# Kernel optimization log

Hardware: AMD Instinct MI355X
Metric: run time of the kernel (lower is better)

## Reference

```python
import jax, jax.numpy as jnp
import numpy as np

QUERY_DIM = 1024
KEY_DIM = 512
HIDDEN_DIM = 128
BATCH = 32
SEQ_LEN = 2048


def setup_inputs() -> dict:
    key = jax.random.key(0)
    k1, k2, k3, k4, k5 = jax.random.split(key, 5)
    query = jax.random.normal(k1, (BATCH, QUERY_DIM), dtype=jnp.float32)
    keys = jax.random.normal(k2, (BATCH, SEQ_LEN, KEY_DIM), dtype=jnp.float32)
    # nn.Linear weights, stored as (out, in) like torch; scaled ~ kaiming-uniform bound
    W1 = jax.random.normal(k3, (HIDDEN_DIM, QUERY_DIM), dtype=jnp.float32) / np.sqrt(QUERY_DIM)
    W2 = jax.random.normal(k4, (HIDDEN_DIM, KEY_DIM), dtype=jnp.float32) / np.sqrt(KEY_DIM)
    V = jax.random.normal(k5, (1, HIDDEN_DIM), dtype=jnp.float32) / np.sqrt(HIDDEN_DIM)
    return {"query": query, "keys": keys, "W1": W1, "W2": W2, "V": V}


def reference(query, keys, W1, W2, V):
    # query: [b, q], keys: [b, s, k]
    q_proj = jnp.einsum("bq,hq->bh", query, W1)          # [b, h]
    k_proj = jnp.einsum("bsk,hk->bsh", keys, W2)          # [b, s, h]
    hidden = jnp.tanh(q_proj[:, None, :] + k_proj)        # [b, s, h]
    score = jnp.einsum("bsh,oh->bs", hidden, V)           # [b, s] (o == 1)
    attention_weights = jax.nn.softmax(score, axis=1)     # [b, s]
    context = jnp.einsum("bs,bsk->bk", attention_weights, keys)  # [b, k]
    return (context, attention_weights)
```

## Files before the change

### kernel.cpp

```cpp
#include <hip/hip_runtime.h>

#define BATCH 32
#define SEQ   2048
#define KD    512
#define QD    1024
#define HD    128

#define NT 16
#define ROWS 64
#define NCHUNK 32

typedef float    f32x4 __attribute__((ext_vector_type(4)));
typedef _Float16 f16x8 __attribute__((ext_vector_type(8)));
typedef unsigned int u32;

__device__ __forceinline__ u32 pack2h(float a, float b) {
    _Float16 ha = (_Float16)a, hb = (_Float16)b;
    unsigned short ua = __builtin_bit_cast(unsigned short, ha);
    unsigned short ub = __builtin_bit_cast(unsigned short, hb);
    return (u32)ua | ((u32)ub << 16);
}

__device__ __forceinline__ void cvt16(const f32x4 a[4], uint4& h0, uint4& h1) {
    h0 = make_uint4(pack2h(a[0][0], a[0][1]), pack2h(a[0][2], a[0][3]),
                    pack2h(a[1][0], a[1][1]), pack2h(a[1][2], a[1][3]));
    h1 = make_uint4(pack2h(a[2][0], a[2][1]), pack2h(a[2][2], a[2][3]),
                    pack2h(a[3][0], a[3][1]), pack2h(a[3][2], a[3][3]));
}

__device__ __forceinline__ f16x8 cvtA(const float4& r0, const float4& r1) {
    uint4 u = make_uint4(pack2h(r0.x, r0.y), pack2h(r0.z, r0.w),
                         pack2h(r1.x, r1.y), pack2h(r1.z, r1.w));
    return __builtin_bit_cast(f16x8, u);
}

__device__ __forceinline__ void gload_lds16(const void* g, void* l) {
    __builtin_amdgcn_global_load_lds(
        (const __attribute__((address_space(1))) unsigned int*)g,
        (__attribute__((address_space(3))) unsigned int*)l, 16, 0, 0);
}

__global__ __launch_bounds__(256) void prep_kernel(
        const float* __restrict__ query, const float* __restrict__ W1,
        const float* __restrict__ W2, float* __restrict__ qp,
        char* __restrict__ w2img) {
    int blk = blockIdx.x;
    int tid = threadIdx.x;
    if (blk < 512) {
        int b = blk >> 4, hg = blk & 15;
        int wave = tid >> 6, lane = tid & 63;
        int h = hg * 8 + wave * 2 + (lane >> 5);
        int l32 = lane & 31;
        const float* q = query + (size_t)b * QD;
        const float* w = W1 + (size_t)h * QD;
        float acc = 0.f;
        #pragma unroll
        for (int i = 0; i < 8; ++i) {
            float4 qv = *(const float4*)(q + i * 128 + l32 * 4);
            float4 wv = *(const float4*)(w + i * 128 + l32 * 4);
            acc += qv.x * wv.x + qv.y * wv.y + qv.z * wv.z + qv.w * wv.w;
        }
        #pragma unroll
        for (int off = 16; off >= 1; off >>= 1) acc += __shfl_xor(acc, off);
        if (l32 == 0) qp[b * HD + h] = acc;
    } else {
        int c = blk - 512;
        int row = tid >> 1;
        int scol = (tid & 1) * 16;
        const float* src = W2 + (size_t)row * KD + c * 32 + scol;
        f32x4 a[4];
        #pragma unroll
        for (int i = 0; i < 4; ++i) a[i] = *(const f32x4*)(src + i * 4);
        uint4 h0, h1;
        cvt16(a, h0, h1);
        int sw = (row & 7) << 4;
        int b0 = c * 8192 + ((row * 64 + scol * 2) ^ sw);
        int b1 = c * 8192 + ((row * 64 + scol * 2 + 16) ^ sw);
        *(uint4*)(w2img + b0) = h0;
        *(uint4*)(w2img + b1) = h1;
    }
}

__global__ __launch_bounds__(256, 4) void score_ctx_kernel(
        const float* __restrict__ keys, const char* __restrict__ w2img,
        const float* __restrict__ qp, const float* __restrict__ V,
        float* __restrict__ score_out, float* __restrict__ part_m,
        float* __restrict__ part_l, float* __restrict__ part_c) {
    __shared__ __align__(16) char Bl[2][8192];
    __shared__ float sc[ROWS];
    __shared__ float pb[ROWS];

    const int blk  = blockIdx.x;
    const int m0   = blk * ROWS;
    const int b    = blk >> 5;
    const int tid  = threadIdx.x;
    const int wave = tid >> 6;
    const int lane = tid & 63;
    const int l15  = lane & 15;
    const int l4   = lane >> 4;

    const float* arow = keys + (size_t)(m0 + wave * 16 + l15) * KD + l4 * 8;
    const int boff0 = (l15 * 64 + l4 * 16) ^ ((l15 & 7) << 4);

    f32x4 acc[8];
    #pragma unroll
    for (int hj = 0; hj < 8; ++hj) acc[hj] = (f32x4)0.f;

    float4 ka[2][2];

#define KA(slot, t) { \
        ka[slot][0] = *(const float4*)(arow + (t) * 32); \
        ka[slot][1] = *(const float4*)(arow + (t) * 32 + 4); }
#define BSTAGE(slot, t) { \
        const char* g_ = w2img + (t) * 8192 + wave * 2048 + lane * 16; \
        gload_lds16(g_,        &Bl[slot][wave * 2048]); \
        gload_lds16(g_ + 1024, &Bl[slot][wave * 2048 + 1024]); }

    BSTAGE(0, 0)
    KA(0, 0)
    __syncthreads();

    #pragma unroll
    for (int t = 0; t < NT; ++t) {
        const int cb = t & 1, nb = cb ^ 1;
        if (t + 1 < NT) {
            BSTAGE(nb, t + 1)
            KA(nb, t + 1)
        }
        f16x8 af = cvtA(ka[cb][0], ka[cb][1]);
        #pragma unroll
        for (int hj = 0; hj < 8; ++hj) {
            f16x8 bh = *(const f16x8*)(&Bl[cb][boff0 + hj * 1024]);
            acc[hj] = __builtin_amdgcn_mfma_f32_16x16x32_f16(af, bh, acc[hj], 0, 0, 0);
        }
        __syncthreads();
    }
#undef KA
#undef BSTAGE

    float qv[8], vv[8];
    #pragma unroll
    for (int hj = 0; hj < 8; ++hj) {
        qv[hj] = qp[b * HD + hj * 16 + l15];
        vv[hj] = V[hj * 16 + l15];
    }

    #pragma unroll
    for (int j = 0; j < 4; ++j) {
        float p = 0.f;
        #pragma unroll
        for (int hj = 0; hj < 8; ++hj) {
            float x = qv[hj] + acc[hj][j];
            float e = __expf(2.f * x);
            float th = 1.f - 2.f * __builtin_amdgcn_rcpf(1.f + e);
            p += th * vv[hj];
        }
        #pragma unroll
        for (int off = 1; off < 16; off <<= 1) p += __shfl_xor(p, off);
        if (l15 == 0) {
            int r = wave * 16 + l4 * 4 + j;
            score_out[m0 + r] = p;
            sc[r] = p;
        }
    }
    __syncthreads();

    float s_val = sc[lane];
    float mx = s_val;
    #pragma unroll
    for (int off = 32; off >= 1; off >>= 1) mx = fmaxf(mx, __shfl_xor(mx, off));
    float p = __expf(s_val - mx);
    float ls = p;
    #pragma unroll
    for (int off = 32; off >= 1; off >>= 1) ls += __shfl_xor(ls, off);
    if (wave == 0) pb[lane] = p;
    if (tid == 0) {
        part_m[blk] = mx;
        part_l[blk] = ls;
    }
    __syncthreads();

    int col = tid * 2;
    float c0 = 0.f, c1 = 0.f;
    const float* kb2 = keys + (size_t)m0 * KD + col;
    #pragma unroll 8
    for (int s = 0; s < ROWS; ++s) {
        float w = pb[s];
        float2 kv = *(const float2*)(kb2 + (size_t)s * KD);
        c0 = fmaf(w, kv.x, c0);
        c1 = fmaf(w, kv.y, c1);
    }
    *(float2*)(part_c + (size_t)blk * KD + col) = make_float2(c0, c1);
}

__global__ __launch_bounds__(256) void finalize_kernel(
        const float* __restrict__ part_m, const float* __restrict__ part_l,
        const float* __restrict__ part_c, float* __restrict__ ctx,
        float* __restrict__ wts) {
    __shared__ float eS[NCHUNK];
    int b = blockIdx.x;
    int tid = threadIdx.x;
    float M = -1e30f;
    #pragma unroll 8
    for (int i = 0; i < NCHUNK; ++i) M = fmaxf(M, part_m[b * NCHUNK + i]);
    if (tid < NCHUNK) eS[tid] = __expf(part_m[b * NCHUNK + tid] - M);
    __syncthreads();
    float L = 0.f;
    #pragma unroll 8
    for (int i = 0; i < NCHUNK; ++i) L += eS[i] * part_l[b * NCHUNK + i];
    float invL = 1.f / L;
    #pragma unroll
    for (int r = 0; r < 8; ++r) {
        int s = tid + r * 256;
        float scv = wts[b * SEQ + s];
        wts[b * SEQ + s] = __expf(scv - M) * invL;
    }
    int col = tid * 2;
    float c0 = 0.f, c1 = 0.f;
    #pragma unroll 8
    for (int i = 0; i < NCHUNK; ++i) {
        float w = eS[i];
        float2 pc = *(const float2*)(part_c + (size_t)(b * NCHUNK + i) * KD + col);
        c0 = fmaf(w, pc.x, c0);
        c1 = fmaf(w, pc.y, c1);
    }
    ctx[b * KD + col]     = c0 * invL;
    ctx[b * KD + col + 1] = c1 * invL;
}

extern "C" void kernel_launch(void* const* d_in, const int* in_sizes, int n_in,
                              void* d_out, int out_size, void* d_ws, size_t ws_size,
                              hipStream_t stream) {
    const float* query = (const float*)d_in[0];
    const float* keys  = (const float*)d_in[1];
    const float* W1    = (const float*)d_in[2];
    const float* W2    = (const float*)d_in[3];
    const float* V     = (const float*)d_in[4];

    float* ctx = (float*)d_out;
    float* wts = (float*)d_out + BATCH * KD;

    char* wsb     = (char*)d_ws;
    float* qp     = (float*)wsb;
    char*  w2img  = wsb + 16 * 1024;
    float* part_m = (float*)(wsb + 144 * 1024);
    float* part_l = (float*)(wsb + 148 * 1024);
    float* part_c = (float*)(wsb + 152 * 1024);

    prep_kernel<<<528, 256, 0, stream>>>(query, W1, W2, qp, w2img);
    score_ctx_kernel<<<BATCH * NCHUNK, 256, 0, stream>>>(
        keys, w2img, qp, V, wts, part_m, part_l, part_c);
    finalize_kernel<<<BATCH, 256, 0, stream>>>(part_m, part_l, part_c, ctx, wts);
}
```

Before: 58.06 us.

## Stage keys tiles through LDS with triple-buffered async loads and single barrier

The keys A-operand now goes global-to-LDS through async global_load_lds with an XOR swizzle, instead of sitting in a register double buffer. Keys and W2 tiles share a three-slot slab so one barrier per iteration is enough, gated by explicit vmcnt waits. The change also raises wave priority around the MFMA block and hoists the qp/V loads. The larger LDS footprint (48KB) lowers the occupancy target from 4 to 3 blocks per CU, and the hand-written waitcnt and barrier logic is fragile.

```diff
diff --git a/kernel.cpp b/kernel.cpp
--- a/kernel.cpp
+++ b/kernel.cpp
@@ -28,9 +28,9 @@
                     pack2h(a[3][0], a[3][1]), pack2h(a[3][2], a[3][3]));
 }
 
-__device__ __forceinline__ f16x8 cvtA(const float4& r0, const float4& r1) {
-    uint4 u = make_uint4(pack2h(r0.x, r0.y), pack2h(r0.z, r0.w),
-                         pack2h(r1.x, r1.y), pack2h(r1.z, r1.w));
+__device__ __forceinline__ f16x8 cvtA4(const f32x4& r0, const f32x4& r1) {
+    uint4 u = make_uint4(pack2h(r0[0], r0[1]), pack2h(r0[2], r0[3]),
+                         pack2h(r1[0], r1[1]), pack2h(r1[2], r1[3]));
     return __builtin_bit_cast(f16x8, u);
 }
 
@@ -81,12 +81,12 @@
     }
 }
 
-__global__ __launch_bounds__(256, 4) void score_ctx_kernel(
+__global__ __launch_bounds__(256, 3) void score_ctx_kernel(
         const float* __restrict__ keys, const char* __restrict__ w2img,
         const float* __restrict__ qp, const float* __restrict__ V,
         float* __restrict__ score_out, float* __restrict__ part_m,
         float* __restrict__ part_l, float* __restrict__ part_c) {
-    __shared__ __align__(16) char Bl[2][8192];
+    __shared__ __align__(16) char slab[3][16384];
     __shared__ float sc[ROWS];
     __shared__ float pb[ROWS];
 
@@ -99,51 +99,59 @@
     const int l15  = lane & 15;
     const int l4   = lane >> 4;
 
-    const float* arow = keys + (size_t)(m0 + wave * 16 + l15) * KD + l4 * 8;
-    const int boff0 = (l15 * 64 + l4 * 16) ^ ((l15 & 7) << 4);
-
-    f32x4 acc[8];
-    #pragma unroll
-    for (int hj = 0; hj < 8; ++hj) acc[hj] = (f32x4)0.f;
-
-    float4 ka[2][2];
-
-#define KA(slot, t) { \
-        ka[slot][0] = *(const float4*)(arow + (t) * 32); \
-        ka[slot][1] = *(const float4*)(arow + (t) * 32 + 4); }
-#define BSTAGE(slot, t) { \
-        const char* g_ = w2img + (t) * 8192 + wave * 2048 + lane * 16; \
-        gload_lds16(g_,        &Bl[slot][wave * 2048]); \
-        gload_lds16(g_ + 1024, &Bl[slot][wave * 2048 + 1024]); }
-
-    BSTAGE(0, 0)
-    KA(0, 0)
-    __syncthreads();
-
-    #pragma unroll
-    for (int t = 0; t < NT; ++t) {
-        const int cb = t & 1, nb = cb ^ 1;
-        if (t + 1 < NT) {
-            BSTAGE(nb, t + 1)
-            KA(nb, t + 1)
-        }
-        f16x8 af = cvtA(ka[cb][0], ka[cb][1]);
-        #pragma unroll
-        for (int hj = 0; hj < 8; ++hj) {
-            f16x8 bh = *(const f16x8*)(&Bl[cb][boff0 + hj * 1024]);
-            acc[hj] = __builtin_amdgcn_mfma_f32_16x16x32_f16(af, bh, acc[hj], 0, 0, 0);
-        }
-        __syncthreads();
-    }
-#undef KA
-#undef BSTAGE
-
     float qv[8], vv[8];
     #pragma unroll
     for (int hj = 0; hj < 8; ++hj) {
         qv[hj] = qp[b * HD + hj * 16 + l15];
         vv[hj] = V[hj * 16 + l15];
     }
+
+    const char* asrc0 = (const char*)keys
+        + (size_t)(m0 + wave * 16 + (lane >> 3)) * (KD * 4)
+        + (((lane & 7) * 16) ^ ((lane >> 3) << 4));
+
+    const int swz = (l15 & 7) << 4;
+    const int ar0 = (wave * 16 + l15) * 128;
+    const int ac0 = (l4 * 32) ^ swz;
+    const int ac1 = (l4 * 32 + 16) ^ swz;
+    const int boff0 = 8192 + ((l15 * 64 + l4 * 16) ^ swz);
+
+    f32x4 acc[8];
+    #pragma unroll
+    for (int hj = 0; hj < 8; ++hj) acc[hj] = (f32x4)0.f;
+
+#define STAGE(slot, t) { \
+        char* as_ = slab[slot]; \
+        gload_lds16(asrc0 + 0 * 16384 + (t) * 128, as_ + wave * 2048 + 0 * 1024); \
+        gload_lds16(asrc0 + 1 * 16384 + (t) * 128, as_ + wave * 2048 + 1 * 1024); \
+        const char* g_ = w2img + (t) * 8192 + wave * 2048 + lane * 16; \
+        gload_lds16(g_,        as_ + 8192 + wave * 2048); \
+        gload_lds16(g_ + 1024, as_ + 8192 + wave * 2048 + 1024); }
+
+    STAGE(0, 0)
+
+    #pragma unroll
+    for (int t = 0; t < NT; ++t) {
+        const int cs = t % 3;
+        if (t + 1 < NT) STAGE((t + 1) % 3, t + 1)
+
+        if (t + 1 < NT) asm volatile("s_waitcnt vmcnt(4)" ::: "memory");
+        else            asm volatile("s_waitcnt vmcnt(0)" ::: "memory");
+        asm volatile("s_barrier" ::: "memory");
+
+        const char* as = slab[cs];
+        f32x4 lo = *(const f32x4*)(as + ar0 + ac0);
+        f32x4 hi = *(const f32x4*)(as + ar0 + ac1);
+        f16x8 af = cvtA4(lo, hi);
+        __builtin_amdgcn_s_setprio(1);
+        #pragma unroll
+        for (int hj = 0; hj < 8; ++hj) {
+            f16x8 bh = *(const f16x8*)(as + boff0 + hj * 1024);
+            acc[hj] = __builtin_amdgcn_mfma_f32_16x16x32_f16(af, bh, acc[hj], 0, 0, 0);
+        }
+        __builtin_amdgcn_s_setprio(0);
+    }
+#undef STAGE
 
     #pragma unroll
     for (int j = 0; j < 4; ++j) {
```

Result: no change. 58.80 us (+1.3%).
